# Kernel tuning notes

Hardware: AMD Instinct MI355X
Metric: run time of the kernel (lower is better)

The kernel has to match this reference:

```python
import jax, jax.numpy as jnp
import numpy as np

EMBED_DIM = 1024
NUM_HEADS = 16
HEAD_DIM = EMBED_DIM // NUM_HEADS
ALPHA = 0.5  # mirror_bias['alpha'] default


def setup_inputs() -> dict:
    key = jax.random.key(0)
    k_x, k_m, kq, kk, kv, ko = jax.random.split(key, 6)
    B, S = 2, 2048
    x = jax.random.normal(k_x, (B, S, EMBED_DIM), dtype=jnp.float32)
    mask = jax.random.bernoulli(k_m, 0.1, (B, S))  # True = masked-out key (padding)
    # xavier_uniform for square [E,E]: limit = sqrt(6/(E+E))
    lim = float(np.sqrt(6.0 / (EMBED_DIM + EMBED_DIM)))
    Wq = jax.random.uniform(kq, (EMBED_DIM, EMBED_DIM), jnp.float32, -lim, lim)
    Wk = jax.random.uniform(kk, (EMBED_DIM, EMBED_DIM), jnp.float32, -lim, lim)
    Wv = jax.random.uniform(kv, (EMBED_DIM, EMBED_DIM), jnp.float32, -lim, lim)
    Wo = jax.random.uniform(ko, (EMBED_DIM, EMBED_DIM), jnp.float32, -lim, lim)
    return {"x": x, "Wq": Wq, "Wk": Wk, "Wv": Wv, "Wo": Wo, "mask": mask}


def _heads(t, B, S):
    # [B,S,E] -> [B,H,S,D]
    return t.reshape(B, S, NUM_HEADS, HEAD_DIM).transpose(0, 2, 1, 3)


def reference(x, Wq, Wk, Wv, Wo, mask):
    B, S, E = x.shape
    # nn.Linear(bias=False): y = x @ W.T
    q = _heads(x @ Wq.T, B, S)
    k = _heads(x @ Wk.T, B, S)
    v = _heads(x @ Wv.T, B, S)
    scores = jnp.einsum('bhqd,bhkd->bhqk', q, k) / jnp.sqrt(jnp.float32(HEAD_DIM))
    # mirror positional bias: target j = S-1-i
    i_idx = jnp.arange(S)[:, None]
    j_idx = jnp.arange(S)[None, :]
    dist = jnp.abs(j_idx - (S - 1 - i_idx)).astype(jnp.float32)
    bias = -ALPHA * (dist / jnp.float32(S))  # [S_q, S_k]
    scores = scores + bias[None, None, :, :]
    # bool 2D mask -> key padding mask [B,1,1,S_k], True = -inf
    scores = jnp.where(mask[:, None, None, :], -jnp.inf, scores)
    attn = jax.nn.softmax(scores, axis=-1)
    out = jnp.einsum('bhqk,bhkd->bhqd', attn, v)
    out = out.transpose(0, 2, 1, 3).reshape(B, S, E)
    return out @ Wo.T
```

## Files before the change

kernel.cpp:

```cpp
#include <hip/hip_runtime.h>

typedef unsigned short u16;
typedef unsigned int u32;
typedef unsigned long long u64;
typedef __attribute__((ext_vector_type(8))) short bf16x8;
typedef __attribute__((ext_vector_type(4))) float f32x4;
typedef __attribute__((ext_vector_type(2))) unsigned int u32x2;
typedef __attribute__((ext_vector_type(4))) unsigned int u32x4;

#define MFMA16(A, B, C) __builtin_amdgcn_mfma_f32_16x16x32_bf16(A, B, C, 0, 0, 0)

__device__ __forceinline__ u16 f2bf(float f) {
  union { float f; unsigned u; } x; x.f = f;
  unsigned r = x.u + 0x7fffu + ((x.u >> 16) & 1u);
  return (u16)(r >> 16);
}

__device__ __forceinline__ u32 pack_bf2(float a, float b) {
  u32 r;
  asm("v_cvt_pk_bf16_f32 %0, %1, %2" : "=v"(r) : "v"(a), "v"(b));
  return r;
}

__device__ __forceinline__ void gload_lds16(const u16* g, u16* l) {
  __builtin_amdgcn_global_load_lds((const __attribute__((address_space(1))) void*)g,
                                   (__attribute__((address_space(3))) void*)l,
                                   16, 0, 0);
}

__global__ __launch_bounds__(256) void cvt_all(const float* __restrict__ x,
                                               const float* __restrict__ Wq,
                                               const float* __restrict__ Wk,
                                               const float* __restrict__ Wv,
                                               const float* __restrict__ Wo,
                                               const int* __restrict__ mask,
                                               u16* __restrict__ xb,
                                               u16* __restrict__ Wqkvb,
                                               u16* __restrict__ Wob,
                                               float* __restrict__ Mbg,
                                               int NE, int NW, int NB) {
  if ((int)blockIdx.x == NB) {
    const int t = threadIdx.x;
    const int j0 = t * 16;
    const float K3C = -8.0f * 1.44269504f;
    const float KMS = K3C - 1.0e6f;
#pragma unroll
    for (int jj = 0; jj < 16; jj += 4) {
      const int4 m4 = *(const int4*)(mask + j0 + jj);
      float4 o;
      o.x = m4.x ? KMS : K3C;
      o.y = m4.y ? KMS : K3C;
      o.z = m4.z ? KMS : K3C;
      o.w = m4.w ? KMS : K3C;
      *(float4*)(Mbg + j0 + jj) = o;
    }
    return;
  }
  const int e = (blockIdx.x * 256 + threadIdx.x) * 8;
  const float* s;
  u16* d;
  if (e < NE) { s = x + e; d = xb + e; }
  else {
    int f = e - NE;
    if (f < 3 * NW) {
      d = Wqkvb + f;
      s = (f < NW) ? Wq + f : (f < 2 * NW) ? Wk + (f - NW) : Wv + (f - 2 * NW);
    } else { f -= 3 * NW; s = Wo + f; d = Wob + f; }
  }
  const float4 a = *(const float4*)s;
  const float4 b = *(const float4*)(s + 4);
  bf16x8 o;
  o[0] = (short)f2bf(a.x); o[1] = (short)f2bf(a.y);
  o[2] = (short)f2bf(a.z); o[3] = (short)f2bf(a.w);
  o[4] = (short)f2bf(b.x); o[5] = (short)f2bf(b.y);
  o[6] = (short)f2bf(b.z); o[7] = (short)f2bf(b.w);
  *(bf16x8*)d = o;
}

__global__ __launch_bounds__(256) void gemm_qkv(const u16* __restrict__ A,
                                                const u16* __restrict__ B,
                                                u16* __restrict__ Qo,
                                                u16* __restrict__ Ko,
                                                u16* __restrict__ Vto,
                                                int M, int N, int K) {
  __shared__ alignas(16) u16 As[128 * 64];
  __shared__ alignas(16) u16 Bs[128 * 64];
  const int t = threadIdx.x;
  const int lane = t & 63, wave = t >> 6;
  const int quad = lane >> 4, l16 = lane & 15;
  const int m0 = blockIdx.y * 128, n0 = blockIdx.x * 128;
  const int wm = (wave >> 1) * 64, wn = (wave & 1) * 64;
  const int sx = l16 & 7;

  f32x4 acc[4][4] = {};

  for (int kk = 0; kk < K; kk += 64) {
#pragma unroll
    for (int i = 0; i < 4; i++) {
      const int c = t + i * 256;
      const int row = c >> 3, sub = c & 7;
      const int col = ((sub ^ (row & 7)) * 8);
      gload_lds16(A + (size_t)(m0 + row) * K + kk + col, As + (size_t)c * 8);
      gload_lds16(B + (size_t)(n0 + row) * K + kk + col, Bs + (size_t)c * 8);
    }
    __syncthreads();

#pragma unroll
    for (int ks = 0; ks < 2; ks++) {
      bf16x8 af[4], bfr[4];
#pragma unroll
      for (int i = 0; i < 4; i++)
        af[i] = *(const bf16x8*)(As + (wm + i * 16 + l16) * 64 +
                                 ((ks * 4 + quad) ^ sx) * 8);
#pragma unroll
      for (int j = 0; j < 4; j++)
        bfr[j] = *(const bf16x8*)(Bs + (wn + j * 16 + l16) * 64 +
                                  ((ks * 4 + quad) ^ sx) * 8);
#pragma unroll
      for (int i = 0; i < 4; i++)
#pragma unroll
        for (int j = 0; j < 4; j++)
          acc[i][j] = MFMA16(af[i], bfr[j], acc[i][j]);
    }
    __syncthreads();
  }

  const int G = ((m0 + wm) & 2047) >> 6;
#pragma unroll
  for (int j = 0; j < 4; j++) {
    const int col = n0 + wn + j * 16 + l16;
    if (col < 1024) {
#pragma unroll
      for (int i = 0; i < 4; i++)
#pragma unroll
        for (int r = 0; r < 4; r++)
          Qo[(size_t)(m0 + wm + i * 16 + quad * 4 + r) * 1024 + col] =
              f2bf(acc[i][j][r]);
    } else if (col < 2048) {
#pragma unroll
      for (int i = 0; i < 4; i++)
#pragma unroll
        for (int r = 0; r < 4; r++)
          Ko[(size_t)(m0 + wm + i * 16 + quad * 4 + r) * 1024 + (col - 1024)] =
              f2bf(acc[i][j][r]);
    } else {
      u16* base = Vto + ((size_t)(m0 >> 11) * 1024 + (col - 2048)) * 2048 + G * 64;
      const int C = 8 * (quad & 1) + 16 * (quad >> 1);
      u32x4 w0, w1;
      w0.x = pack_bf2(acc[0][j][0], acc[0][j][1]);
      w0.y = pack_bf2(acc[0][j][2], acc[0][j][3]);
      w0.z = pack_bf2(acc[1][j][0], acc[1][j][1]);
      w0.w = pack_bf2(acc[1][j][2], acc[1][j][3]);
      w1.x = pack_bf2(acc[2][j][0], acc[2][j][1]);
      w1.y = pack_bf2(acc[2][j][2], acc[2][j][3]);
      w1.z = pack_bf2(acc[3][j][0], acc[3][j][1]);
      w1.w = pack_bf2(acc[3][j][2], acc[3][j][3]);
      *(u32x4*)(base + C) = w0;
      *(u32x4*)(base + C + 32) = w1;
    }
  }
}

__global__ __launch_bounds__(256) void gemm_out(const u16* __restrict__ A,
                                                const u16* __restrict__ B,
                                                float* __restrict__ C,
                                                int M, int N, int K) {
  __shared__ alignas(16) u16 As[128 * 64];
  __shared__ alignas(16) u16 Bs[64 * 64];
  const int t = threadIdx.x;
  const int lane = t & 63, wave = t >> 6;
  const int quad = lane >> 4, l16 = lane & 15;
  const int m0 = blockIdx.y * 128, n0 = blockIdx.x * 64;
  const int wm = (wave >> 1) * 64, wn = (wave & 1) * 32;
  const int sx = l16 & 7;

  f32x4 acc[4][2] = {};

  for (int kk = 0; kk < K; kk += 64) {
#pragma unroll
    for (int i = 0; i < 4; i++) {
      const int c = t + i * 256;
      const int row = c >> 3, sub = c & 7;
      gload_lds16(A + (size_t)(m0 + row) * K + kk + ((sub ^ (row & 7)) * 8),
                  As + (size_t)c * 8);
    }
#pragma unroll
    for (int i = 0; i < 2; i++) {
      const int c = t + i * 256;
      const int row = c >> 3, sub = c & 7;
      gload_lds16(B + (size_t)(n0 + row) * K + kk + ((sub ^ (row & 7)) * 8),
                  Bs + (size_t)c * 8);
    }
    __syncthreads();

#pragma unroll
    for (int ks = 0; ks < 2; ks++) {
      bf16x8 af[4], bfr[2];
#pragma unroll
      for (int i = 0; i < 4; i++)
        af[i] = *(const bf16x8*)(As + (wm + i * 16 + l16) * 64 +
                                 ((ks * 4 + quad) ^ sx) * 8);
#pragma unroll
      for (int j = 0; j < 2; j++)
        bfr[j] = *(const bf16x8*)(Bs + (wn + j * 16 + l16) * 64 +
                                  ((ks * 4 + quad) ^ sx) * 8);
#pragma unroll
      for (int i = 0; i < 4; i++)
#pragma unroll
        for (int j = 0; j < 2; j++)
          acc[i][j] = MFMA16(af[i], bfr[j], acc[i][j]);
    }
    __syncthreads();
  }

#pragma unroll
  for (int i = 0; i < 4; i++)
#pragma unroll
    for (int j = 0; j < 2; j++)
#pragma unroll
      for (int r = 0; r < 4; r++)
        C[(size_t)(m0 + wm + i * 16 + quad * 4 + r) * N + n0 + wn + j * 16 + l16] =
            acc[i][j][r];
}

__global__ __launch_bounds__(256) void attn_fwd(const u16* __restrict__ Q,
                                                const u16* __restrict__ Kb_,
                                                const u16* __restrict__ Vt,
                                                const float* __restrict__ Mb,
                                                float* __restrict__ OP0,
                                                float* __restrict__ OP1,
                                                float* __restrict__ Lp) {
  constexpr int S = 2048, E = 1024;
  __shared__ alignas(16) u16 Ks[2][64 * 64];
  __shared__ alignas(16) u16 Vs[2][64 * 64];
  const int t = threadIdx.x;
  const int lane = t & 63, wave = t >> 6;
  const int quad = lane >> 4, l16 = lane & 15;
  const int bh = blockIdx.y, b = bh >> 4, h = bh & 15;
  const int sp = blockIdx.z;
  const int kbase0 = sp * 1024;
  const int q0 = blockIdx.x * 128 + wave * 32;

  const int c0 = t, c1 = t + 256;
  const int kr0 = c0 >> 3, kr1 = c1 >> 3;
  const int kcol0 = ((c0 & 7) ^ (kr0 & 7)) * 8;
  const int kcol1 = ((c1 & 7) ^ (kr1 & 7)) * 8;
  const u16* kP0 = Kb_ + (size_t)(b * S + kbase0 + kr0) * E + h * 64 + kcol0;
  const u16* kP1 = Kb_ + (size_t)(b * S + kbase0 + kr1) * E + h * 64 + kcol1;
  const u16* vbase = Vt + (size_t)(b * 16 + h) * 64 * S + kbase0;
  const u16* vP0 = vbase + (size_t)kr0 * S + kcol0;
  const u16* vP1 = vbase + (size_t)kr1 * S + kcol1;

  bf16x8 aq[2][2];
#pragma unroll
  for (int qt = 0; qt < 2; qt++) {
    const u16* qp = Q + ((size_t)(b * S) + q0 + qt * 16 + l16) * E + h * 64;
    aq[qt][0] = *(const bf16x8*)(qp + quad * 8);
    aq[qt][1] = *(const bf16x8*)(qp + 32 + quad * 8);
  }

  const float* mbp = Mb + b * 2048 + kbase0 + quad * 4;
  const int sx = l16 & 7;

  float lr[2] = {};
  f32x4 accO[2][4] = {};
  const float fb0 = (float)(kbase0 + quad * 4 + q0 + l16 - 2047);

  const float K1 = 0.125f * 1.44269504f;
  const float K2 = 2.44140625e-4f * 1.44269504f;

  gload_lds16(kP0, Ks[0] + c0 * 8);
  gload_lds16(kP1, Ks[0] + c1 * 8);
  gload_lds16(vP0, Vs[0] + c0 * 8);
  gload_lds16(vP1, Vs[0] + c1 * 8);
  __syncthreads();

  int buf = 0;
  for (int kc = 0; kc < 1024; kc += 64) {
    if (kc + 64 < 1024) {
      const int kn = kc + 64;
      gload_lds16(kP0 + (size_t)kn * E, Ks[buf ^ 1] + c0 * 8);
      gload_lds16(kP1 + (size_t)kn * E, Ks[buf ^ 1] + c1 * 8);
      gload_lds16(vP0 + kn, Vs[buf ^ 1] + c0 * 8);
      gload_lds16(vP1 + kn, Vs[buf ^ 1] + c1 * 8);
    }
    f32x4 mv[4];
#pragma unroll
    for (int T = 0; T < 4; T++) mv[T] = *(const f32x4*)(mbp + kc + 16 * T);

    const u16* ks = Ks[buf];
    const u16* vs = Vs[buf];

    bf16x8 bk[4][2];
#pragma unroll
    for (int T = 0; T < 4; T++)
#pragma unroll
      for (int dh = 0; dh < 2; dh++)
        bk[T][dh] = *(const bf16x8*)(ks + (T * 16 + l16) * 64 +
                                     ((dh * 4 + quad) ^ sx) * 8);

    f32x4 s[2][4] = {};
    __builtin_amdgcn_s_setprio(1);
#pragma unroll
    for (int qt = 0; qt < 2; qt++)
#pragma unroll
      for (int T = 0; T < 4; T++) {
        s[qt][T] = MFMA16(bk[T][0], aq[qt][0], s[qt][T]);
        s[qt][T] = MFMA16(bk[T][1], aq[qt][1], s[qt][T]);
      }
    __builtin_amdgcn_s_setprio(0);

    const float fbL = fb0 + (float)kc;

    u32 pw[2][2][4];
#pragma unroll
    for (int qt = 0; qt < 2; qt++)
#pragma unroll
      for (int T = 0; T < 4; T++) {
        float p[4];
#pragma unroll
        for (int r = 0; r < 4; r++) {
          const float fe = fbL + (float)(16 * T + 16 * qt + r);
          const float tv = fmaf(s[qt][T][r], K1, mv[T][r]);
          p[r] = __builtin_amdgcn_exp2f(fmaf(fabsf(fe), -K2, tv));
        }
        lr[qt] += (p[0] + p[1]) + (p[2] + p[3]);
        pw[qt][T >> 1][(T & 1) * 2 + 0] = pack_bf2(p[0], p[1]);
        pw[qt][T >> 1][(T & 1) * 2 + 1] = pack_bf2(p[2], p[3]);
      }

    __builtin_amdgcn_s_setprio(1);
#pragma unroll
    for (int kst = 0; kst < 2; kst++) {
      bf16x8 bv[4];
#pragma unroll
      for (int tt = 0; tt < 4; tt++)
        bv[tt] = *(const bf16x8*)(vs + (tt * 16 + l16) * 64 +
                                  ((kst * 4 + quad) ^ sx) * 8);
#pragma unroll
      for (int qt = 0; qt < 2; qt++) {
        union { u32 w[4]; bf16x8 v; } ap;
        ap.w[0] = pw[qt][kst][0]; ap.w[1] = pw[qt][kst][1];
        ap.w[2] = pw[qt][kst][2]; ap.w[3] = pw[qt][kst][3];
#pragma unroll
        for (int tt = 0; tt < 4; tt++)
          accO[qt][tt] = MFMA16(ap.v, bv[tt], accO[qt][tt]);
      }
    }
    __builtin_amdgcn_s_setprio(0);

    __syncthreads();
    buf ^= 1;
  }

  float* OP = sp ? OP1 : OP0;
#pragma unroll
  for (int qt = 0; qt < 2; qt++) {
    float l = lr[qt];
    l += __shfl_xor(l, 16);
    l += __shfl_xor(l, 32);
    if (lane < 16)
      Lp[((size_t)sp << 16) + ((size_t)bh << 11) + q0 + qt * 16 + l16] = l;
  }
#pragma unroll
  for (int qt = 0; qt < 2; qt++)
#pragma unroll
    for (int r = 0; r < 4; r++) {
      const int qg = q0 + qt * 16 + quad * 4 + r;
      const size_t row = ((size_t)bh << 11) + qg;
      float* orow = OP + row * 64;
#pragma unroll
      for (int tt = 0; tt < 4; tt++) orow[tt * 16 + l16] = accO[qt][tt][r];
    }
}

__global__ __launch_bounds__(256) void attn_merge(const float* __restrict__ OP0,
                                                  const float* __restrict__ OP1,
                                                  const float* __restrict__ Lp,
                                                  u16* __restrict__ Ao) {
  const int i = blockIdx.x * 256 + threadIdx.x;
  const int row = i >> 4;
  const int d4 = (i & 15) * 4;
  const float inv = 1.0f / (Lp[row] + Lp[65536 + row]);
  const float4 a = *(const float4*)(OP0 + (size_t)row * 64 + d4);
  const float4 c = *(const float4*)(OP1 + (size_t)row * 64 + d4);
  const int bb = row >> 15, h = (row >> 11) & 15, q = row & 2047;
  u32x2 v;
  v.x = pack_bf2((a.x + c.x) * inv, (a.y + c.y) * inv);
  v.y = pack_bf2((a.z + c.z) * inv, (a.w + c.w) * inv);
  *(u32x2*)(Ao + (size_t)((bb << 11) + q) * 1024 + h * 64 + d4) = v;
}

extern "C" void kernel_launch(void* const* d_in, const int* in_sizes, int n_in,
                              void* d_out, int out_size, void* d_ws, size_t ws_size,
                              hipStream_t stream) {
  const float* x  = (const float*)d_in[0];
  const float* Wq = (const float*)d_in[1];
  const float* Wk = (const float*)d_in[2];
  const float* Wv = (const float*)d_in[3];
  const float* Wo = (const float*)d_in[4];
  const int* mask = (const int*)d_in[5];

  const int M = 4096, N = 1024, K = 1024;
  const int NE = M * N, NW = N * K;
  const int NB = (NE + 4 * NW) / 2048;

  u16* xb    = (u16*)d_ws;
  u16* Wqkvb = xb + NE;
  u16* Wob   = Wqkvb + (size_t)3 * NW;
  u16* Qb    = Wob + NW;
  u16* Kb    = Qb + NE;
  u16* Vt    = Kb + NE;
  u16* Ao    = Vt + NE;
  float* Mbg = (float*)(Ao + NE);
  float* OP1 = Mbg + 4096;
  float* Lp  = OP1 + (size_t)65536 * 64;
  float* OP0 = (float*)d_out;

  cvt_all<<<NB + 1, 256, 0, stream>>>(x, Wq, Wk, Wv, Wo, mask,
                                      xb, Wqkvb, Wob, Mbg, NE, NW, NB);

  gemm_qkv<<<dim3(3072 / 128, M / 128), 256, 0, stream>>>(
      xb, Wqkvb, Qb, Kb, Vt, M, 3072, K);
  attn_fwd<<<dim3(16, 32, 2), 256, 0, stream>>>(Qb, Kb, Vt, Mbg,
                                                OP0, OP1, Lp);
  attn_merge<<<4096, 256, 0, stream>>>(OP0, OP1, Lp, Ao);
  gemm_out<<<dim3(N / 64, M / 128), 256, 0, stream>>>(
      Ao, Wob, (float*)d_out, M, N, K);
}
```

Before: 202.1 us.

## Swizzle block IDs across XCDs, stage mask bias in LDS, drop setprio

All three main kernels now use a flattened 1D grid with an XCD-aware block-ID remap, so blocks that share operand tiles run on the same XCD and reuse its L2. The attention kernel loads its 1024-entry mask-bias slice into shared memory once per block instead of reading it from global memory every iteration. The s_setprio hints around the MFMA sections are removed. The remap adds a little integer arithmetic per block, and removing the priority hints could change how waves interleave.

Result: faster. 194.4 us (-3.8%).

```diff
diff --git a/kernel.cpp b/kernel.cpp
--- a/kernel.cpp
+++ b/kernel.cpp
@@ -88,7 +88,9 @@
   const int t = threadIdx.x;
   const int lane = t & 63, wave = t >> 6;
   const int quad = lane >> 4, l16 = lane & 15;
-  const int m0 = blockIdx.y * 128, n0 = blockIdx.x * 128;
+  const int bid = blockIdx.x;
+  const int swz = (bid & 7) * 96 + (bid >> 3);
+  const int m0 = (swz / 24) * 128, n0 = (swz % 24) * 128;
   const int wm = (wave >> 1) * 64, wn = (wave & 1) * 64;
   const int sx = l16 & 7;
 
@@ -170,7 +172,9 @@
   const int t = threadIdx.x;
   const int lane = t & 63, wave = t >> 6;
   const int quad = lane >> 4, l16 = lane & 15;
-  const int m0 = blockIdx.y * 128, n0 = blockIdx.x * 64;
+  const int bid = blockIdx.x;
+  const int swz = (bid & 7) * 64 + (bid >> 3);
+  const int m0 = (swz >> 4) * 128, n0 = (swz & 15) * 64;
   const int wm = (wave >> 1) * 64, wn = (wave & 1) * 32;
   const int sx = l16 & 7;
 
@@ -233,13 +237,16 @@
   constexpr int S = 2048, E = 1024;
   __shared__ alignas(16) u16 Ks[2][64 * 64];
   __shared__ alignas(16) u16 Vs[2][64 * 64];
+  __shared__ alignas(16) float Ms[1024];
   const int t = threadIdx.x;
   const int lane = t & 63, wave = t >> 6;
   const int quad = lane >> 4, l16 = lane & 15;
-  const int bh = blockIdx.y, b = bh >> 4, h = bh & 15;
-  const int sp = blockIdx.z;
+  const int bid = blockIdx.x;
+  const int swz = (bid & 7) * 128 + (bid >> 3);
+  const int xq = swz & 15, bh = (swz >> 4) & 31, sp = swz >> 9;
+  const int b = bh >> 4, h = bh & 15;
   const int kbase0 = sp * 1024;
-  const int q0 = blockIdx.x * 128 + wave * 32;
+  const int q0 = xq * 128 + wave * 32;
 
   const int c0 = t, c1 = t + 256;
   const int kr0 = c0 >> 3, kr1 = c1 >> 3;
@@ -259,7 +266,6 @@
     aq[qt][1] = *(const bf16x8*)(qp + 32 + quad * 8);
   }
 
-  const float* mbp = Mb + b * 2048 + kbase0 + quad * 4;
   const int sx = l16 & 7;
 
   float lr[2] = {};
@@ -273,6 +279,8 @@
   gload_lds16(kP1, Ks[0] + c1 * 8);
   gload_lds16(vP0, Vs[0] + c0 * 8);
   gload_lds16(vP1, Vs[0] + c1 * 8);
+  gload_lds16((const u16*)(Mb + b * 2048 + kbase0) + t * 8,
+              (u16*)Ms + t * 8);
   __syncthreads();
 
   int buf = 0;
@@ -284,12 +292,13 @@
       gload_lds16(vP0 + kn, Vs[buf ^ 1] + c0 * 8);
       gload_lds16(vP1 + kn, Vs[buf ^ 1] + c1 * 8);
     }
-    f32x4 mv[4];
-#pragma unroll
-    for (int T = 0; T < 4; T++) mv[T] = *(const f32x4*)(mbp + kc + 16 * T);
-
     const u16* ks = Ks[buf];
     const u16* vs = Vs[buf];
+
+    f32x4 mv[4];
+#pragma unroll
+    for (int T = 0; T < 4; T++)
+      mv[T] = *(const f32x4*)(Ms + kc + 16 * T + quad * 4);
 
     bf16x8 bk[4][2];
 #pragma unroll
@@ -300,7 +309,6 @@
                                      ((dh * 4 + quad) ^ sx) * 8);
 
     f32x4 s[2][4] = {};
-    __builtin_amdgcn_s_setprio(1);
 #pragma unroll
     for (int qt = 0; qt < 2; qt++)
 #pragma unroll
@@ -308,7 +316,6 @@
         s[qt][T] = MFMA16(bk[T][0], aq[qt][0], s[qt][T]);
         s[qt][T] = MFMA16(bk[T][1], aq[qt][1], s[qt][T]);
       }
-    __builtin_amdgcn_s_setprio(0);
 
     const float fbL = fb0 + (float)kc;
 
@@ -329,7 +336,6 @@
         pw[qt][T >> 1][(T & 1) * 2 + 1] = pack_bf2(p[2], p[3]);
       }
 
-    __builtin_amdgcn_s_setprio(1);
 #pragma unroll
     for (int kst = 0; kst < 2; kst++) {
       bf16x8 bv[4];
@@ -347,7 +353,6 @@
           accO[qt][tt] = MFMA16(ap.v, bv[tt], accO[qt][tt]);
       }
     }
-    __builtin_amdgcn_s_setprio(0);
 
     __syncthreads();
     buf ^= 1;
@@ -420,11 +425,8 @@
   cvt_all<<<NB + 1, 256, 0, stream>>>(x, Wq, Wk, Wv, Wo, mask,
                                       xb, Wqkvb, Wob, Mbg, NE, NW, NB);
 
-  gemm_qkv<<<dim3(3072 / 128, M / 128), 256, 0, stream>>>(
-      xb, Wqkvb, Qb, Kb, Vt, M, 3072, K);
-  attn_fwd<<<dim3(16, 32, 2), 256, 0, stream>>>(Qb, Kb, Vt, Mbg,
-                                                OP0, OP1, Lp);
+  gemm_qkv<<<768, 256, 0, stream>>>(xb, Wqkvb, Qb, Kb, Vt, M, 3072, K);
+  attn_fwd<<<1024, 256, 0, stream>>>(Qb, Kb, Vt, Mbg, OP0, OP1, Lp);
   attn_merge<<<4096, 256, 0, stream>>>(OP0, OP1, Lp, Ao);
-  gemm_out<<<dim3(N / 64, M / 128), 256, 0, stream>>>(
-      Ao, Wob, (float*)d_out, M, N, K);
-}
+  gemm_out<<<512, 256, 0, stream>>>(Ao, Wob, (float*)d_out, M, N, K);
+}
```
